# Optimization experiments

Hardware: AMD Instinct MI355X
Metric: run time of the kernel (lower is better)

## Reference

```python
import jax, jax.numpy as jnp
import numpy as np

EPS = 1e-5
IOU_SCALE = 10000.0
NEG_TH_ACGT = 3000.0   # int(10000*0.3)
POS_TH_ACGT = 5000.0   # int(10000*0.5)
NUM_POS_RPN = 128
NUM_NEG_RPN = 128

B, N_AC, N_GT = 8, 128 * 128 * 9, 64


def _make_boxes(u):
    # u in [0,1): (yc, xc, sh, sw) -> valid YXYX boxes
    yc, xc = u[..., 0], u[..., 1]
    hh = 0.05 + 0.25 * u[..., 2]
    ww = 0.05 + 0.25 * u[..., 3]
    return jnp.stack([yc - 0.5 * hh, xc - 0.5 * ww, yc + 0.5 * hh, xc + 0.5 * ww], axis=-1)


def setup_inputs() -> dict:
    key = jax.random.key(0)
    k1, k2, k3 = jax.random.split(key, 3)
    anchors = _make_boxes(jax.random.uniform(k1, (N_AC, 4)))
    gt_boxes = _make_boxes(jax.random.uniform(k2, (B, N_GT, 4)))
    deltas = 0.1 * jax.random.normal(k3, (B, N_AC, 4), dtype=jnp.float32)
    return {"anchors": anchors, "gt_boxes": gt_boxes, "deltas": deltas}


def _area(b):
    return jnp.maximum(b[..., 2] - b[..., 0], 0.0) * jnp.maximum(b[..., 3] - b[..., 1], 0.0)


def _iou(ac, gt):
    # ac: (A,4), gt: (B,G,4) -> scaled IoU (B,A,G)
    a = ac[None, :, None, :]
    g = gt[:, None, :, :]
    yi = jnp.maximum(a[..., 0], g[..., 0])
    xi = jnp.maximum(a[..., 1], g[..., 1])
    ya = jnp.minimum(a[..., 2], g[..., 2])
    xa = jnp.minimum(a[..., 3], g[..., 3])
    inter = jnp.maximum(ya - yi, 0.0) * jnp.maximum(xa - xi, 0.0)
    union = _area(a) + _area(g) - inter
    return IOU_SCALE * inter / (union + EPS)


def _bbox2delta(bl, br):
    wr, hr = br[..., 3] - br[..., 1], br[..., 2] - br[..., 0]
    xcr, ycr = br[..., 1] + 0.5 * wr, br[..., 0] + 0.5 * hr
    wr_c, hr_c = jnp.maximum(wr, EPS), jnp.maximum(hr, EPS)
    wl, hl = bl[..., 3] - bl[..., 1], bl[..., 2] - bl[..., 0]
    xcl, ycl = bl[..., 1] + 0.5 * wl, bl[..., 0] + 0.5 * hl
    d = jnp.stack([(xcl - xcr) / wr_c, (ycl - ycr) / hr_c,
                   jnp.log(wl / wr_c), jnp.log(hl / hr_c)], axis=-1)
    return jnp.clip(d, -10.0, 10.0)


def _delta2bbox(base, diff):
    wb, hb = base[..., 3] - base[..., 1], base[..., 2] - base[..., 0]
    xc = base[..., 1] + 0.5 * wb + wb * diff[..., 0]
    yc = base[..., 0] + 0.5 * hb + hb * diff[..., 1]
    w_ = wb * jnp.exp(diff[..., 2])
    h_ = hb * jnp.exp(diff[..., 3])
    # from_xywh -> YXYX
    return jnp.stack([yc - 0.5 * h_, xc - 0.5 * w_, yc + 0.5 * h_, xc + 0.5 * w_], axis=-1)


def _sample_mask(mask, num, key):
    th = num / (jnp.sum(mask, axis=-1, keepdims=True) + 1e-6)
    rand = jax.random.uniform(key, mask.shape, dtype=jnp.float32)
    return jnp.where(rand < th, 1.0, 0.0) * mask


def reference(anchors, gt_boxes, deltas):
    ious = _iou(anchors, gt_boxes)                 # (B, A, G)
    best_iou = jnp.max(ious, axis=-1)              # (B, A)
    best_idx = jnp.argmax(ious, axis=-1)           # (B, A)
    gt_best = jnp.take_along_axis(
        gt_boxes, jnp.broadcast_to(best_idx[:, :, None], best_idx.shape + (4,)), axis=1)

    pos = best_iou > POS_TH_ACGT
    neg = best_iou < NEG_TH_ACGT
    # fg: matched GT box; bkg: all -2; ignore: all -1
    bx_tgt = jnp.where(pos[..., None], gt_best,
                       jnp.where(neg[..., None], -2.0, -1.0))

    coor_sum = jnp.sum(bx_tgt, axis=-1)
    kp, kn = jax.random.split(jax.random.key(42))
    mask_pos = _sample_mask(jnp.where(coor_sum > -4.0, 1.0, 0.0), NUM_POS_RPN, kp)
    mask_neg = _sample_mask(jnp.where(coor_sum <= -8.0, 1.0, 0.0), NUM_NEG_RPN, kn)

    ac_b = jnp.broadcast_to(anchors[None], bx_tgt.shape)
    # safe left operand so log() stays finite for non-positive anchors
    bx_tgt_safe = jnp.where(pos[..., None], bx_tgt, ac_b)
    del_tgt = _bbox2delta(bx_tgt_safe, ac_b) * mask_pos[..., None]   # (B, A, 4)

    proposals = _delta2bbox(anchors[None], deltas)                    # (B, A, 4)
    return jnp.concatenate([proposals, del_tgt], axis=-1)            # (B, A, 8)
```

## Files before the change

kernel.cpp:

```cpp
#include <hip/hip_runtime.h>
#include <stdint.h>

#define NAC 147456
#define NGT 64
#define NB  8
#define APT 3
#define BLK 256
#define GX  (NAC / (BLK * APT))
#define LCAP 36864

__host__ __device__ static inline uint32_t tf_rotl(uint32_t x, uint32_t d) {
  return (x << d) | (x >> (32u - d));
}

__host__ __device__ static inline void threefry2x32(
    uint32_t k0, uint32_t k1, uint32_t x0, uint32_t x1,
    uint32_t* o0, uint32_t* o1)
{
  const uint32_t ks2 = k0 ^ k1 ^ 0x1BD11BDAu;
  x0 += k0; x1 += k1;
#define TFR(r) { x0 += x1; x1 = tf_rotl(x1, (r)); x1 ^= x0; }
  TFR(13u) TFR(15u) TFR(26u) TFR(6u)   x0 += k1;  x1 += ks2 + 1u;
  TFR(17u) TFR(29u) TFR(16u) TFR(24u)  x0 += ks2; x1 += k0 + 2u;
  TFR(13u) TFR(15u) TFR(26u) TFR(6u)   x0 += k0;  x1 += k1 + 3u;
  TFR(17u) TFR(29u) TFR(16u) TFR(24u)  x0 += k1;  x1 += ks2 + 4u;
  TFR(13u) TFR(15u) TFR(26u) TFR(6u)   x0 += ks2; x1 += k0 + 5u;
#undef TFR
  *o0 = x0; *o1 = x1;
}

__device__ static inline void bbox2delta_store(
    const float4& a, const float4& g, float* dst)
{
  const float wr  = a.w - a.y,          hr  = a.z - a.x;
  const float xcr = a.y + 0.5f * wr,    ycr = a.x + 0.5f * hr;
  const float wrc = fmaxf(wr, 1e-5f),   hrc = fmaxf(hr, 1e-5f);
  const float wl  = g.w - g.y,          hl  = g.z - g.x;
  const float xcl = g.y + 0.5f * wl,    ycl = g.x + 0.5f * hl;
  float4 r;
  r.x = fminf(fmaxf((xcl - xcr) / wrc, -10.0f), 10.0f);
  r.y = fminf(fmaxf((ycl - ycr) / hrc, -10.0f), 10.0f);
  r.z = fminf(fmaxf(__logf(wl / wrc),  -10.0f), 10.0f);
  r.w = fminf(fmaxf(__logf(hl / hrc),  -10.0f), 10.0f);
  *reinterpret_cast<float4*>(dst) = r;
}

template <bool USE_LIST>
__global__ __launch_bounds__(BLK) void k1_classify(
    const float* __restrict__ anchors,
    const float* __restrict__ gt,
    const float* __restrict__ deltas,
    float* __restrict__ out,
    int* __restrict__ cnt,
    uint32_t* __restrict__ list)
{
  __shared__ __align__(16) float4 gbox[NGT];
  __shared__ __align__(16) float  garea[NGT];
  __shared__ __align__(16) float  gae[NGT];
  __shared__ int s_cnt;
  __shared__ int s_base;
  const int b   = blockIdx.y;
  const int tid = threadIdx.x;

  if (tid == 0) s_cnt = 0;
  if (tid < NGT) {
    float4 g = reinterpret_cast<const float4*>(gt)[b * NGT + tid];
    const float ga = fmaxf(g.z - g.x, 0.0f) * fmaxf(g.w - g.y, 0.0f);
    gbox[tid]  = g;
    garea[tid] = ga;
    gae[tid]   = ga + 1e-5f;
  }
  __syncthreads();

  const int base = blockIdx.x * (BLK * APT) + tid;

  float4 a[APT];
  float  areaA[APT], num[APT], Tb[APT];
  int    bidx[APT];
#pragma unroll
  for (int t = 0; t < APT; ++t) {
    a[t] = reinterpret_cast<const float4*>(anchors)[base + t * BLK];
    areaA[t] = fmaxf(a[t].z - a[t].x, 0.0f) * fmaxf(a[t].w - a[t].y, 0.0f);
    num[t]  = 0.0f;
    Tb[t]   = 1.0f;
    bidx[t] = 0;
  }

  for (int jj = 0; jj < NGT; jj += 4) {
    const float4 te4 = *reinterpret_cast<const float4*>(&gae[jj]);
    const float4 g0 = gbox[jj + 0];
    const float4 g1 = gbox[jj + 1];
    const float4 g2 = gbox[jj + 2];
    const float4 g3 = gbox[jj + 3];
    const float4 gs[4] = { g0, g1, g2, g3 };
#pragma unroll
    for (int u = 0; u < 4; ++u) {
      const float4 g  = gs[u];
      const float  te = (&te4.x)[u];
      const int    j  = jj + u;
#pragma unroll
      for (int t = 0; t < APT; ++t) {
        float yi = fmaxf(a[t].x, g.x);
        float xi = fmaxf(a[t].y, g.y);
        float ya = fminf(a[t].z, g.z);
        float xa = fminf(a[t].w, g.w);
        float inter = fmaxf(ya - yi, 0.0f) * (xa - xi);
        float Tj = areaA[t] + te;
        bool upd = inter * Tb[t] > num[t] * Tj;
        num[t]  = upd ? inter : num[t];
        Tb[t]   = upd ? Tj    : Tb[t];
        bidx[t] = upd ? j     : bidx[t];
      }
    }
  }

  int slot[APT];
#pragma unroll
  for (int t = 0; t < APT; ++t) {
    const int i = base + t * BLK;
    const float gaB = garea[bidx[t]];
    const float den = ((areaA[t] + gaB) - num[t]) + 1e-5f;
    const float best_iou = (10000.0f * num[t]) / den;
    const bool pos = best_iou > 5000.0f;
    slot[t] = pos ? atomicAdd(&s_cnt, 1) : -1;

    const float4 d = reinterpret_cast<const float4*>(deltas)[b * NAC + i];
    const float wb = a[t].w - a[t].y, hb = a[t].z - a[t].x;
    const float xc = a[t].y + 0.5f * wb + wb * d.x;
    const float yc = a[t].x + 0.5f * hb + hb * d.y;
    const float w_ = wb * __expf(d.z);
    const float h_ = hb * __expf(d.w);

    float* rowp = out + ((size_t)b * NAC + i) * 8;
    reinterpret_cast<float4*>(rowp)[0] =
        make_float4(yc - 0.5f * h_, xc - 0.5f * w_, yc + 0.5f * h_, xc + 0.5f * w_);
    if (USE_LIST) {
      reinterpret_cast<float4*>(rowp)[1] = make_float4(0.f, 0.f, 0.f, 0.f);
    } else {
      reinterpret_cast<float4*>(rowp)[1] =
          make_float4(pos ? (float)(bidx[t] + 1) : 0.0f, 0.f, 0.f, 0.f);
    }
  }
  __syncthreads();
  if (tid == 0) {
    s_base = s_cnt ? atomicAdd(&cnt[b], s_cnt) : 0;
  }
  __syncthreads();

  if (USE_LIST) {
#pragma unroll
    for (int t = 0; t < APT; ++t) {
      if (slot[t] >= 0) {
        const int e = s_base + slot[t];
        if (e < LCAP) {
          const int i = base + t * BLK;
          list[b * LCAP + e] = (uint32_t)i | ((uint32_t)bidx[t] << 18);
        }
      }
    }
  }
}

__global__ __launch_bounds__(256) void k2_list(
    const float* __restrict__ anchors,
    const float* __restrict__ gt,
    float* __restrict__ out,
    const int* __restrict__ cnt,
    const uint32_t* __restrict__ list,
    uint32_t kp0, uint32_t kp1)
{
  const int b   = blockIdx.y;
  const int tid = threadIdx.x;

  int tot = cnt[b];
  const float th = 128.0f / ((float)tot + 1e-6f);
  if (tot > LCAP) tot = LCAP;

  for (int e = blockIdx.x * 256 + tid; e < tot; e += 16 * 256) {
    const uint32_t p = list[b * LCAP + e];
    const int i  = (int)(p & 0x3FFFFu);
    const int fl = (int)(p >> 18);
    const int f  = b * NAC + i;

    uint32_t o0, o1;
    threefry2x32(kp0, kp1, 0u, (uint32_t)f, &o0, &o1);
    const uint32_t bits = o0 ^ o1;
    union { uint32_t u; float flt; } cv;
    cv.u = (bits >> 9) | 0x3F800000u;
    if (cv.flt - 1.0f < th) {
      const float4 a = reinterpret_cast<const float4*>(anchors)[i];
      const float4 g = reinterpret_cast<const float4*>(gt)[b * NGT + fl];
      bbox2delta_store(a, g, out + (size_t)f * 8 + 4);
    }
  }
}

__global__ __launch_bounds__(256) void k2_fallback(
    const float* __restrict__ anchors,
    const float* __restrict__ gt,
    float* __restrict__ out,
    const int* __restrict__ counts,
    uint32_t kp0, uint32_t kp1)
{
  const int b = blockIdx.y;
  const int i = blockIdx.x * 256 + threadIdx.x;
  const int f = b * NAC + i;
  float* rowp = out + (size_t)f * 8;

  const float flag = rowp[4];
  if (flag == 0.0f) return;

  const float th = 128.0f / ((float)counts[b] + 1e-6f);

  uint32_t o0, o1;
  threefry2x32(kp0, kp1, 0u, (uint32_t)f, &o0, &o1);
  const uint32_t bits = o0 ^ o1;
  union { uint32_t u; float flt; } cv;
  cv.u = (bits >> 9) | 0x3F800000u;

  if (cv.flt - 1.0f < th) {
    const float4 a = reinterpret_cast<const float4*>(anchors)[i];
    const float4 g = reinterpret_cast<const float4*>(gt)[b * NGT + ((int)flag - 1)];
    bbox2delta_store(a, g, rowp + 4);
  } else {
    reinterpret_cast<float4*>(rowp)[1] = make_float4(0.f, 0.f, 0.f, 0.f);
  }
}

extern "C" void kernel_launch(void* const* d_in, const int* in_sizes, int n_in,
                              void* d_out, int out_size, void* d_ws, size_t ws_size,
                              hipStream_t stream)
{
  const float* anchors = (const float*)d_in[0];
  const float* gt      = (const float*)d_in[1];
  const float* deltas  = (const float*)d_in[2];
  float* out  = (float*)d_out;
  int* cnt = (int*)d_ws;
  uint32_t* list = (uint32_t*)((char*)d_ws + 256);

  const bool use_list = ws_size >= (size_t)(256 + NB * LCAP * 4);

  uint32_t kp0, kp1;
  threefry2x32(0u, 42u, 0u, 0u, &kp0, &kp1);

  hipMemsetAsync(cnt, 0, NB * sizeof(int), stream);

  dim3 g1(GX, NB);
  if (use_list) {
    k1_classify<true><<<g1, dim3(BLK), 0, stream>>>(anchors, gt, deltas, out,
                                                    cnt, list);
    dim3 g2(16, NB);
    k2_list<<<g2, dim3(256), 0, stream>>>(anchors, gt, out, cnt, list,
                                          kp0, kp1);
  } else {
    k1_classify<false><<<g1, dim3(BLK), 0, stream>>>(anchors, gt, deltas, out,
                                                     cnt, nullptr);
    dim3 g2(NAC / 256, NB);
    k2_fallback<<<g2, dim3(256), 0, stream>>>(anchors, gt, out, cnt,
                                              kp0, kp1);
  }
}
```

Measured before the change: 115.1 us.

## Replace global atomic list with per-block segments and drop memset launch

Each classify block now writes its positive count and its compact list into a private fixed-size segment instead of reserving space with a global atomic. The second kernel sums the per-block counts itself, so the memset launch and the cross-block atomic go away. The second kernel now runs as one block per batch, with one thread walking each segment serially, which cuts its parallelism. Segments are capped at 160 entries, so a block with more positives than that would silently drop some.

```diff
diff --git a/kernel.cpp b/kernel.cpp
--- a/kernel.cpp
+++ b/kernel.cpp
@@ -7,7 +7,7 @@
 #define APT 3
 #define BLK 256
 #define GX  (NAC / (BLK * APT))
-#define LCAP 36864
+#define SEGCAP 160
 
 __host__ __device__ static inline uint32_t tf_rotl(uint32_t x, uint32_t d) {
   return (x << d) | (x >> (32u - d));
@@ -51,14 +51,13 @@
     const float* __restrict__ gt,
     const float* __restrict__ deltas,
     float* __restrict__ out,
-    int* __restrict__ cnt,
+    int* __restrict__ cnt_blk,
     uint32_t* __restrict__ list)
 {
   __shared__ __align__(16) float4 gbox[NGT];
   __shared__ __align__(16) float  garea[NGT];
   __shared__ __align__(16) float  gae[NGT];
   __shared__ int s_cnt;
-  __shared__ int s_base;
   const int b   = blockIdx.y;
   const int tid = threadIdx.x;
 
@@ -142,55 +141,61 @@
     }
   }
   __syncthreads();
-  if (tid == 0) {
-    s_base = s_cnt ? atomicAdd(&cnt[b], s_cnt) : 0;
-  }
-  __syncthreads();
 
   if (USE_LIST) {
+    if (tid == 0)
+      cnt_blk[b * GX + blockIdx.x] = s_cnt;
+    uint32_t* seg = list + ((size_t)(b * GX + blockIdx.x)) * SEGCAP;
 #pragma unroll
     for (int t = 0; t < APT; ++t) {
-      if (slot[t] >= 0) {
-        const int e = s_base + slot[t];
-        if (e < LCAP) {
-          const int i = base + t * BLK;
-          list[b * LCAP + e] = (uint32_t)i | ((uint32_t)bidx[t] << 18);
-        }
+      if (slot[t] >= 0 && slot[t] < SEGCAP) {
+        const int i = base + t * BLK;
+        seg[slot[t]] = (uint32_t)i | ((uint32_t)bidx[t] << 18);
       }
     }
-  }
-}
-
-__global__ __launch_bounds__(256) void k2_list(
+  } else {
+    if (tid == 0 && s_cnt) atomicAdd(&cnt_blk[b], s_cnt);
+  }
+}
+
+__global__ __launch_bounds__(256) void k2_seg(
     const float* __restrict__ anchors,
     const float* __restrict__ gt,
     float* __restrict__ out,
-    const int* __restrict__ cnt,
+    const int* __restrict__ cnt_blk,
     const uint32_t* __restrict__ list,
     uint32_t kp0, uint32_t kp1)
 {
+  __shared__ int s_tot;
   const int b   = blockIdx.y;
   const int tid = threadIdx.x;
 
-  int tot = cnt[b];
-  const float th = 128.0f / ((float)tot + 1e-6f);
-  if (tot > LCAP) tot = LCAP;
-
-  for (int e = blockIdx.x * 256 + tid; e < tot; e += 16 * 256) {
-    const uint32_t p = list[b * LCAP + e];
-    const int i  = (int)(p & 0x3FFFFu);
-    const int fl = (int)(p >> 18);
-    const int f  = b * NAC + i;
-
-    uint32_t o0, o1;
-    threefry2x32(kp0, kp1, 0u, (uint32_t)f, &o0, &o1);
-    const uint32_t bits = o0 ^ o1;
-    union { uint32_t u; float flt; } cv;
-    cv.u = (bits >> 9) | 0x3F800000u;
-    if (cv.flt - 1.0f < th) {
-      const float4 a = reinterpret_cast<const float4*>(anchors)[i];
-      const float4 g = reinterpret_cast<const float4*>(gt)[b * NGT + fl];
-      bbox2delta_store(a, g, out + (size_t)f * 8 + 4);
+  if (tid == 0) s_tot = 0;
+  __syncthreads();
+  const int c = (tid < GX) ? cnt_blk[b * GX + tid] : 0;
+  if (c) atomicAdd(&s_tot, c);
+  __syncthreads();
+  const float th = 128.0f / ((float)s_tot + 1e-6f);
+
+  if (tid < GX) {
+    const uint32_t* seg = list + ((size_t)(b * GX + tid)) * SEGCAP;
+    const int n = (c < SEGCAP) ? c : SEGCAP;
+    for (int k = 0; k < n; ++k) {
+      const uint32_t p = seg[k];
+      const int i  = (int)(p & 0x3FFFFu);
+      const int fl = (int)(p >> 18);
+      const int f  = b * NAC + i;
+
+      uint32_t o0, o1;
+      threefry2x32(kp0, kp1, 0u, (uint32_t)f, &o0, &o1);
+      const uint32_t bits = o0 ^ o1;
+      union { uint32_t u; float flt; } cv;
+      cv.u = (bits >> 9) | 0x3F800000u;
+      if (cv.flt - 1.0f < th) {
+        const float4 a = reinterpret_cast<const float4*>(anchors)[i];
+        const float4 g = reinterpret_cast<const float4*>(gt)[b * NGT + fl];
+        bbox2delta_store(a, g, out + (size_t)f * 8 + 4);
+      }
     }
   }
 }
@@ -235,28 +240,27 @@
   const float* gt      = (const float*)d_in[1];
   const float* deltas  = (const float*)d_in[2];
   float* out  = (float*)d_out;
-  int* cnt = (int*)d_ws;
-  uint32_t* list = (uint32_t*)((char*)d_ws + 256);
-
-  const bool use_list = ws_size >= (size_t)(256 + NB * LCAP * 4);
+  int* cnt_blk = (int*)d_ws;
+  uint32_t* list = (uint32_t*)((char*)d_ws + 8192);
+
+  const bool use_list = ws_size >= (size_t)(8192 + (size_t)NB * GX * SEGCAP * 4);
 
   uint32_t kp0, kp1;
   threefry2x32(0u, 42u, 0u, 0u, &kp0, &kp1);
-
-  hipMemsetAsync(cnt, 0, NB * sizeof(int), stream);
 
   dim3 g1(GX, NB);
   if (use_list) {
     k1_classify<true><<<g1, dim3(BLK), 0, stream>>>(anchors, gt, deltas, out,
-                                                    cnt, list);
-    dim3 g2(16, NB);
-    k2_list<<<g2, dim3(256), 0, stream>>>(anchors, gt, out, cnt, list,
-                                          kp0, kp1);
+                                                    cnt_blk, list);
+    dim3 g2(1, NB);
+    k2_seg<<<g2, dim3(256), 0, stream>>>(anchors, gt, out, cnt_blk, list,
+                                         kp0, kp1);
   } else {
+    hipMemsetAsync(cnt_blk, 0, NB * sizeof(int), stream);
     k1_classify<false><<<g1, dim3(BLK), 0, stream>>>(anchors, gt, deltas, out,
-                                                     cnt, nullptr);
+                                                     cnt_blk, nullptr);
     dim3 g2(NAC / 256, NB);
-    k2_fallback<<<g2, dim3(256), 0, stream>>>(anchors, gt, out, cnt,
+    k2_fallback<<<g2, dim3(256), 0, stream>>>(anchors, gt, out, cnt_blk,
                                               kp0, kp1);
   }
 }
```

Result: slower. 166.5 us (+44.7%).
